# Optimization experiments

Hardware: AMD Instinct MI355X
Metric: run time of the kernel (lower is better)

The kernel has to match this reference:

```python
import jax, jax.numpy as jnp
import numpy as np

SIGMA = 5.67e-8  # Stefan-Boltzmann constant
NX = 13
N = NX * NX  # 169 nodes
B = 131072


def _build_matrices(L=0.1, thickness=0.001, board_k=15.0, emis=0.8):
    dx = L / (NX - 1)
    dy = L / (NX - 1)
    GLx = thickness * board_k * dy / dx
    GLy = thickness * board_k * dx / dy
    GR = 2.0 * dx * dy * emis
    iface = {0, NX - 1, NX * NX - 1, NX * NX - NX}
    K = np.zeros((N, N), dtype=np.float32)
    for j in range(NX):
        for i in range(NX):
            idn = i + NX * j
            if idn in iface:
                K[idn, idn] = 1.0
            else:
                gii = 0.0
                if i + 1 < NX:
                    K[idn, idn + 1] = -GLx  # east
                    gii += GLx
                if i - 1 >= 0:
                    K[idn, idn - 1] = -GLx  # west
                    gii += GLx
                if j + 1 < NX:
                    K[idn, idn + NX] = -GLx  # north (original code uses -GLx here too)
                    gii += GLy
                if j - 1 >= 0:
                    K[idn, idn - NX] = -GLx  # south (original code uses -GLx here too)
                    gii += GLy
                K[idn, idn] = gii
    e = np.full(N, GR, dtype=np.float32)
    for t in iface:
        e[t] = 0.0
    return jnp.asarray(K), jnp.asarray(e)


def setup_inputs() -> dict:
    key = jax.random.key(0)
    k1, k2, k3, k4 = jax.random.split(key, 4)
    # realistic temperatures (K) and heat loads (W)
    outputs = 270.0 + 60.0 * jax.random.uniform(k1, (B, NX, NX), dtype=jnp.float32)
    heaters = 0.5 * jax.random.uniform(k2, (B, NX, NX), dtype=jnp.float32)
    interfaces = 0.5 * jax.random.uniform(k3, (B, NX, NX), dtype=jnp.float32)
    Tenv = 270.0 + 30.0 * jax.random.uniform(k4, (B, 1), dtype=jnp.float32)
    K, e_diag = _build_matrices()
    return {"outputs": outputs, "heaters": heaters, "interfaces": interfaces,
            "Tenv": Tenv, "K": K, "e_diag": e_diag}


def reference(outputs, heaters, interfaces, Tenv, K, e_diag):
    b = outputs.shape[0]
    T = outputs.reshape(b, -1)                    # [B, 169]
    Q = heaters.reshape(b, -1) + interfaces.reshape(b, -1)  # [B, 169]
    # original computes K @ T_nodes_x_batch; batch-major equivalent is T @ K^T
    conduction = jnp.einsum('bn,mn->bm', T, K)    # [B, 169]
    radiation = SIGMA * e_diag[None, :] * (T ** 4 - Tenv ** 4)  # Tenv [B,1] broadcasts
    excess = conduction + radiation - Q
    return jnp.mean(jnp.abs(excess))
```

## Files before the change

kernel.cpp:

```cpp
#include <hip/hip_runtime.h>
#include <math.h>


#define SIGMA_F 5.67e-8f

constexpr int BLOCK = 256;

typedef float f4a __attribute__((ext_vector_type(4), aligned(4)));
typedef float f4b __attribute__((ext_vector_type(4), aligned(16)));

__global__ __launch_bounds__(256) void fused_residual_v4(
    const float* __restrict__ T,
    const float* __restrict__ H,
    const float* __restrict__ F,
    const float* __restrict__ Tenv,
    const float* __restrict__ K,
    const float* __restrict__ Ediag,
    float* __restrict__ partials,
    int total)
{
    __shared__ float sred[BLOCK / 64];

    const float GLx = -K[1 * 169 + 2];
    const float GRs = SIGMA_F * Ediag[1];

    const int lane = threadIdx.x & 63;
    float acc = 0.0f;

    const int gstride = gridDim.x * BLOCK;
    for (int g = blockIdx.x * BLOCK + threadIdx.x; g * 8 < total; g += gstride) {
        const int e0 = g * 8;
        const int waveBase = e0 - lane * 8;
        const bool fast = (waveBase >= 16) && (waveBase + 64 * 8 + 16 <= total);

        if (fast) {
            f4b t0 = *(const f4b*)(T + e0);
            f4b t1 = *(const f4b*)(T + e0 + 4);
            f4b h0 = __builtin_nontemporal_load((const f4b*)(H + e0));
            f4b h1 = __builtin_nontemporal_load((const f4b*)(H + e0 + 4));
            f4b f0 = __builtin_nontemporal_load((const f4b*)(F + e0));
            f4b f1 = __builtin_nontemporal_load((const f4b*)(F + e0 + 4));

            float sv[8];
            sv[0] = __shfl_up(t0.w, 2);
            sv[1] = __shfl_up(t1.x, 2);
            sv[2] = __shfl_up(t1.y, 2);
            sv[3] = __shfl_up(t1.z, 2);
            sv[4] = __shfl_up(t1.w, 2);
            sv[5] = __shfl_up(t0.x, 1);
            sv[6] = __shfl_up(t0.y, 1);
            sv[7] = __shfl_up(t0.z, 1);
            if (lane < 2) {
                f4a a = *(const f4a*)(T + e0 - 13);
                f4a b = *(const f4a*)(T + e0 - 9);
                sv[0] = a.x; sv[1] = a.y; sv[2] = a.z; sv[3] = a.w;
                sv[4] = b.x; sv[5] = b.y; sv[6] = b.z; sv[7] = b.w;
            }
            float nv[8];
            nv[0] = __shfl_down(t1.y, 1);
            nv[1] = __shfl_down(t1.z, 1);
            nv[2] = __shfl_down(t1.w, 1);
            nv[3] = __shfl_down(t0.x, 2);
            nv[4] = __shfl_down(t0.y, 2);
            nv[5] = __shfl_down(t0.z, 2);
            nv[6] = __shfl_down(t0.w, 2);
            nv[7] = __shfl_down(t1.x, 2);
            if (lane >= 62) {
                f4a a = *(const f4a*)(T + e0 + 13);
                f4a b = *(const f4a*)(T + e0 + 17);
                nv[0] = a.x; nv[1] = a.y; nv[2] = a.z; nv[3] = a.w;
                nv[4] = b.x; nv[5] = b.y; nv[6] = b.z; nv[7] = b.w;
            }
            float left = __shfl_up(t1.w, 1);
            if (lane == 0) left = T[e0 - 1];
            float right = __shfl_down(t0.x, 1);
            if (lane == 63) right = T[e0 + 8];

            unsigned ue = (unsigned)e0;
            unsigned b0 = ue / 169u;
            int m0 = (int)(ue - b0 * 169u);
            unsigned q13 = (unsigned)m0 / 13u;
            int i0 = m0 - (int)q13 * 13;

            float tvA = Tenv[b0];
            float tvB = tvA;
            if (m0 >= 162) tvB = Tenv[b0 + 1];
            float tv4A = (tvA * tvA) * (tvA * tvA);
            float tv4B = (tvB * tvB) * (tvB * tvB);

            const float tC[8] = {t0.x, t0.y, t0.z, t0.w, t1.x, t1.y, t1.z, t1.w};
            const float tW[8] = {left, t0.x, t0.y, t0.z, t0.w, t1.x, t1.y, t1.z};
            const float tE[8] = {t0.y, t0.z, t0.w, t1.x, t1.y, t1.z, t1.w, right};
            const float hq[8] = {h0.x + f0.x, h0.y + f0.y, h0.z + f0.z, h0.w + f0.w,
                                 h1.x + f1.x, h1.y + f1.y, h1.z + f1.z, h1.w + f1.w};

            int m = m0, ii = i0;
            bool wrapped = false;
            #pragma unroll
            for (int j = 0; j < 8; ++j) {
                float t = tC[j];
                bool cE = (ii < 12), cW = (ii > 0), cN = (m < 156), cS = (m >= 13);
                bool ifc = (m == 0) | (m == 12) | (m == 156) | (m == 168);
                float s  = (cE ? tE[j] : 0.0f) + (cW ? tW[j] : 0.0f)
                         + (cN ? nv[j] : 0.0f) + (cS ? sv[j] : 0.0f);
                float nn = (cE ? 1.0f : 0.0f) + (cW ? 1.0f : 0.0f)
                         + (cN ? 1.0f : 0.0f) + (cS ? 1.0f : 0.0f);
                float t2 = t * t, t4 = t2 * t2;
                float tv4 = wrapped ? tv4B : tv4A;
                float ex = ifc ? (t - hq[j])
                               : (GLx * (nn * t - s) + GRs * (t4 - tv4) - hq[j]);
                acc += fabsf(ex);
                ++m; ++ii;
                if (ii == 13) ii = 0;
                if (m == 169) { m = 0; ii = 0; wrapped = true; }
            }
        } else {
            #pragma unroll
            for (int j = 0; j < 8; ++j) {
                int e = e0 + j;
                if (e >= total) break;
                unsigned b = (unsigned)e / 169u;
                int m = e - (int)b * 169;
                unsigned q13 = (unsigned)m / 13u;
                int ii = m - (int)q13 * 13;
                bool cE = (ii < 12), cW = (ii > 0), cN = (m < 156), cS = (m >= 13);
                bool ifc = (m == 0) | (m == 12) | (m == 156) | (m == 168);
                float t  = T[e];
                float tEv = cE ? T[e + 1]  : 0.0f;
                float tWv = cW ? T[e - 1]  : 0.0f;
                float tNv = cN ? T[e + 13] : 0.0f;
                float tSv = cS ? T[e - 13] : 0.0f;
                float s  = tEv + tWv + tNv + tSv;
                float nn = (float)((int)cE + (int)cW + (int)cN + (int)cS);
                float tv = Tenv[b];
                float tv4 = (tv * tv) * (tv * tv);
                float t2 = t * t, t4 = t2 * t2;
                float q = H[e] + F[e];
                float ex = ifc ? (t - q)
                               : (GLx * (nn * t - s) + GRs * (t4 - tv4) - q);
                acc += fabsf(ex);
            }
        }
    }

    #pragma unroll
    for (int off = 32; off > 0; off >>= 1)
        acc += __shfl_down(acc, off, 64);
    int wid = threadIdx.x >> 6;
    if (lane == 0) sred[wid] = acc;
    __syncthreads();
    if (threadIdx.x == 0) {
        float s = 0.0f;
        #pragma unroll
        for (int w = 0; w < BLOCK / 64; ++w) s += sred[w];
        partials[blockIdx.x] = s;
    }
}

__global__ __launch_bounds__(256) void finalize_kernel(
    const float* __restrict__ partials, int n,
    float* __restrict__ out, float inv_total)
{
    __shared__ float sred[BLOCK / 64];
    float acc = 0.0f;
    for (int i = (int)threadIdx.x; i < n; i += BLOCK) acc += partials[i];
    #pragma unroll
    for (int off = 32; off > 0; off >>= 1)
        acc += __shfl_down(acc, off, 64);
    int lane = threadIdx.x & 63;
    int wid  = threadIdx.x >> 6;
    if (lane == 0) sred[wid] = acc;
    __syncthreads();
    if (threadIdx.x == 0) {
        float s = 0.0f;
        #pragma unroll
        for (int w = 0; w < BLOCK / 64; ++w) s += sred[w];
        out[0] = s * inv_total;
    }
}

extern "C" void kernel_launch(void* const* d_in, const int* in_sizes, int n_in,
                              void* d_out, int out_size, void* d_ws, size_t ws_size,
                              hipStream_t stream) {
    const float* T    = (const float*)d_in[0];
    const float* H    = (const float*)d_in[1];
    const float* F    = (const float*)d_in[2];
    const float* Tenv = (const float*)d_in[3];
    const float* K    = (const float*)d_in[4];
    const float* E    = (const float*)d_in[5];
    float* out      = (float*)d_out;
    float* partials = (float*)d_ws;

    const int total = in_sizes[0];

    int grid = (total / 8 + BLOCK - 1) / BLOCK;
    if ((size_t)grid * sizeof(float) > ws_size) grid = (int)(ws_size / sizeof(float));
    if (grid < 1) grid = 1;

    fused_residual_v4<<<grid, BLOCK, 0, stream>>>(T, H, F, Tenv, K, E, partials, total);

    const float inv_total = 1.0f / (float)total;
    finalize_kernel<<<1, BLOCK, 0, stream>>>(partials, grid, out, inv_total);
}
```

Baseline: 245.7 us.

## Assign one 13-element grid row per thread with direct neighbor-row loads

```diff
diff --git a/kernel.cpp b/kernel.cpp
--- a/kernel.cpp
+++ b/kernel.cpp
@@ -7,9 +7,8 @@
 constexpr int BLOCK = 256;
 
 typedef float f4a __attribute__((ext_vector_type(4), aligned(4)));
-typedef float f4b __attribute__((ext_vector_type(4), aligned(16)));
 
-__global__ __launch_bounds__(256) void fused_residual_v4(
+__global__ __launch_bounds__(256) void fused_residual_v5(
     const float* __restrict__ T,
     const float* __restrict__ H,
     const float* __restrict__ F,
@@ -17,136 +16,106 @@
     const float* __restrict__ K,
     const float* __restrict__ Ediag,
     float* __restrict__ partials,
-    int total)
+    int rows)
 {
     __shared__ float sred[BLOCK / 64];
 
     const float GLx = -K[1 * 169 + 2];
     const float GRs = SIGMA_F * Ediag[1];
 
-    const int lane = threadIdx.x & 63;
     float acc = 0.0f;
 
     const int gstride = gridDim.x * BLOCK;
-    for (int g = blockIdx.x * BLOCK + threadIdx.x; g * 8 < total; g += gstride) {
-        const int e0 = g * 8;
-        const int waveBase = e0 - lane * 8;
-        const bool fast = (waveBase >= 16) && (waveBase + 64 * 8 + 16 <= total);
+    for (int r = blockIdx.x * BLOCK + (int)threadIdx.x; r < rows; r += gstride) {
+        const unsigned ur = (unsigned)r;
+        const unsigned b  = ur / 13u;
+        const int j = (int)(ur - b * 13u);
+        const bool cS = (j > 0), cN = (j < 12);
+        const float fS = cS ? 1.0f : 0.0f;
+        const float fN = cN ? 1.0f : 0.0f;
 
-        if (fast) {
-            f4b t0 = *(const f4b*)(T + e0);
-            f4b t1 = *(const f4b*)(T + e0 + 4);
-            f4b h0 = __builtin_nontemporal_load((const f4b*)(H + e0));
-            f4b h1 = __builtin_nontemporal_load((const f4b*)(H + e0 + 4));
-            f4b f0 = __builtin_nontemporal_load((const f4b*)(F + e0));
-            f4b f1 = __builtin_nontemporal_load((const f4b*)(F + e0 + 4));
+        const int e0 = r * 13;
+        const float* Tp = T + e0;
+        const float* Sp = T + (cS ? e0 - 13 : e0);
+        const float* Np = T + (cN ? e0 + 13 : e0);
 
-            float sv[8];
-            sv[0] = __shfl_up(t0.w, 2);
-            sv[1] = __shfl_up(t1.x, 2);
-            sv[2] = __shfl_up(t1.y, 2);
-            sv[3] = __shfl_up(t1.z, 2);
-            sv[4] = __shfl_up(t1.w, 2);
-            sv[5] = __shfl_up(t0.x, 1);
-            sv[6] = __shfl_up(t0.y, 1);
-            sv[7] = __shfl_up(t0.z, 1);
-            if (lane < 2) {
-                f4a a = *(const f4a*)(T + e0 - 13);
-                f4a b = *(const f4a*)(T + e0 - 9);
-                sv[0] = a.x; sv[1] = a.y; sv[2] = a.z; sv[3] = a.w;
-                sv[4] = b.x; sv[5] = b.y; sv[6] = b.z; sv[7] = b.w;
-            }
-            float nv[8];
-            nv[0] = __shfl_down(t1.y, 1);
-            nv[1] = __shfl_down(t1.z, 1);
-            nv[2] = __shfl_down(t1.w, 1);
-            nv[3] = __shfl_down(t0.x, 2);
-            nv[4] = __shfl_down(t0.y, 2);
-            nv[5] = __shfl_down(t0.z, 2);
-            nv[6] = __shfl_down(t0.w, 2);
-            nv[7] = __shfl_down(t1.x, 2);
-            if (lane >= 62) {
-                f4a a = *(const f4a*)(T + e0 + 13);
-                f4a b = *(const f4a*)(T + e0 + 17);
-                nv[0] = a.x; nv[1] = a.y; nv[2] = a.z; nv[3] = a.w;
-                nv[4] = b.x; nv[5] = b.y; nv[6] = b.z; nv[7] = b.w;
-            }
-            float left = __shfl_up(t1.w, 1);
-            if (lane == 0) left = T[e0 - 1];
-            float right = __shfl_down(t0.x, 1);
-            if (lane == 63) right = T[e0 + 8];
+        f4a tA = *(const f4a*)(Tp);
+        f4a tB = *(const f4a*)(Tp + 4);
+        f4a tC = *(const f4a*)(Tp + 8);
+        float t12 = Tp[12];
+        f4a sA = *(const f4a*)(Sp);
+        f4a sB = *(const f4a*)(Sp + 4);
+        f4a sC = *(const f4a*)(Sp + 8);
+        float s12 = Sp[12];
+        f4a nA = *(const f4a*)(Np);
+        f4a nB = *(const f4a*)(Np + 4);
+        f4a nC = *(const f4a*)(Np + 8);
+        float n12 = Np[12];
+        f4a hA = __builtin_nontemporal_load((const f4a*)(H + e0));
+        f4a hB = __builtin_nontemporal_load((const f4a*)(H + e0 + 4));
+        f4a hC = __builtin_nontemporal_load((const f4a*)(H + e0 + 8));
+        float h12 = __builtin_nontemporal_load(H + e0 + 12);
+        f4a fA = __builtin_nontemporal_load((const f4a*)(F + e0));
+        f4a fB = __builtin_nontemporal_load((const f4a*)(F + e0 + 4));
+        f4a fC = __builtin_nontemporal_load((const f4a*)(F + e0 + 8));
+        float f12 = __builtin_nontemporal_load(F + e0 + 12);
 
-            unsigned ue = (unsigned)e0;
-            unsigned b0 = ue / 169u;
-            int m0 = (int)(ue - b0 * 169u);
-            unsigned q13 = (unsigned)m0 / 13u;
-            int i0 = m0 - (int)q13 * 13;
+        const float tv  = Tenv[b];
+        const float tv2 = tv * tv;
+        const float nGtv4 = -(GRs * (tv2 * tv2));
 
-            float tvA = Tenv[b0];
-            float tvB = tvA;
-            if (m0 >= 162) tvB = Tenv[b0 + 1];
-            float tv4A = (tvA * tvA) * (tvA * tvA);
-            float tv4B = (tvB * tvB) * (tvB * tvB);
+        const float tR[13] = {tA.x, tA.y, tA.z, tA.w, tB.x, tB.y, tB.z, tB.w,
+                              tC.x, tC.y, tC.z, tC.w, t12};
+        const float sR[13] = {sA.x, sA.y, sA.z, sA.w, sB.x, sB.y, sB.z, sB.w,
+                              sC.x, sC.y, sC.z, sC.w, s12};
+        const float nR[13] = {nA.x, nA.y, nA.z, nA.w, nB.x, nB.y, nB.z, nB.w,
+                              nC.x, nC.y, nC.z, nC.w, n12};
+        const float qR[13] = {hA.x + fA.x, hA.y + fA.y, hA.z + fA.z, hA.w + fA.w,
+                              hB.x + fB.x, hB.y + fB.y, hB.z + fB.z, hB.w + fB.w,
+                              hC.x + fC.x, hC.y + fC.y, hC.z + fC.z, hC.w + fC.w,
+                              h12 + f12};
 
-            const float tC[8] = {t0.x, t0.y, t0.z, t0.w, t1.x, t1.y, t1.z, t1.w};
-            const float tW[8] = {left, t0.x, t0.y, t0.z, t0.w, t1.x, t1.y, t1.z};
-            const float tE[8] = {t0.y, t0.z, t0.w, t1.x, t1.y, t1.z, t1.w, right};
-            const float hq[8] = {h0.x + f0.x, h0.y + f0.y, h0.z + f0.z, h0.w + f0.w,
-                                 h1.x + f1.x, h1.y + f1.y, h1.z + f1.z, h1.w + f1.w};
+        const float nnI = 2.0f + fN + fS;
+        const float nnE = 1.0f + fN + fS;
+        const bool ifc = (j == 0) | (j == 12);
 
-            int m = m0, ii = i0;
-            bool wrapped = false;
-            #pragma unroll
-            for (int j = 0; j < 8; ++j) {
-                float t = tC[j];
-                bool cE = (ii < 12), cW = (ii > 0), cN = (m < 156), cS = (m >= 13);
-                bool ifc = (m == 0) | (m == 12) | (m == 156) | (m == 168);
-                float s  = (cE ? tE[j] : 0.0f) + (cW ? tW[j] : 0.0f)
-                         + (cN ? nv[j] : 0.0f) + (cS ? sv[j] : 0.0f);
-                float nn = (cE ? 1.0f : 0.0f) + (cW ? 1.0f : 0.0f)
-                         + (cN ? 1.0f : 0.0f) + (cS ? 1.0f : 0.0f);
-                float t2 = t * t, t4 = t2 * t2;
-                float tv4 = wrapped ? tv4B : tv4A;
-                float ex = ifc ? (t - hq[j])
-                               : (GLx * (nn * t - s) + GRs * (t4 - tv4) - hq[j]);
-                acc += fabsf(ex);
-                ++m; ++ii;
-                if (ii == 13) ii = 0;
-                if (m == 169) { m = 0; ii = 0; wrapped = true; }
-            }
-        } else {
-            #pragma unroll
-            for (int j = 0; j < 8; ++j) {
-                int e = e0 + j;
-                if (e >= total) break;
-                unsigned b = (unsigned)e / 169u;
-                int m = e - (int)b * 169;
-                unsigned q13 = (unsigned)m / 13u;
-                int ii = m - (int)q13 * 13;
-                bool cE = (ii < 12), cW = (ii > 0), cN = (m < 156), cS = (m >= 13);
-                bool ifc = (m == 0) | (m == 12) | (m == 156) | (m == 168);
-                float t  = T[e];
-                float tEv = cE ? T[e + 1]  : 0.0f;
-                float tWv = cW ? T[e - 1]  : 0.0f;
-                float tNv = cN ? T[e + 13] : 0.0f;
-                float tSv = cS ? T[e - 13] : 0.0f;
-                float s  = tEv + tWv + tNv + tSv;
-                float nn = (float)((int)cE + (int)cW + (int)cN + (int)cS);
-                float tv = Tenv[b];
-                float tv4 = (tv * tv) * (tv * tv);
-                float t2 = t * t, t4 = t2 * t2;
-                float q = H[e] + F[e];
-                float ex = ifc ? (t - q)
-                               : (GLx * (nn * t - s) + GRs * (t4 - tv4) - q);
-                acc += fabsf(ex);
-            }
+        {
+            float t = tR[0];
+            float s = tR[1];
+            s = fmaf(fN, nR[0], s);
+            s = fmaf(fS, sR[0], s);
+            float t2 = t * t;
+            float ex = fmaf(GLx, fmaf(nnE, t, -s), fmaf(GRs, t2 * t2, nGtv4)) - qR[0];
+            float exI = t - qR[0];
+            acc += fabsf(ifc ? exI : ex);
+        }
+        #pragma unroll
+        for (int i = 1; i < 12; ++i) {
+            float t = tR[i];
+            float s = tR[i - 1] + tR[i + 1];
+            s = fmaf(fN, nR[i], s);
+            s = fmaf(fS, sR[i], s);
+            float t2 = t * t;
+            float ex = fmaf(GLx, fmaf(nnI, t, -s), fmaf(GRs, t2 * t2, nGtv4)) - qR[i];
+            acc += fabsf(ex);
+        }
+        {
+            float t = tR[12];
+            float s = tR[11];
+            s = fmaf(fN, nR[12], s);
+            s = fmaf(fS, sR[12], s);
+            float t2 = t * t;
+            float ex = fmaf(GLx, fmaf(nnE, t, -s), fmaf(GRs, t2 * t2, nGtv4)) - qR[12];
+            float exI = t - qR[12];
+            acc += fabsf(ifc ? exI : ex);
         }
     }
 
     #pragma unroll
     for (int off = 32; off > 0; off >>= 1)
         acc += __shfl_down(acc, off, 64);
-    int wid = threadIdx.x >> 6;
+    const int lane = threadIdx.x & 63;
+    const int wid  = threadIdx.x >> 6;
     if (lane == 0) sred[wid] = acc;
     __syncthreads();
     if (threadIdx.x == 0) {
@@ -192,12 +161,13 @@
     float* partials = (float*)d_ws;
 
     const int total = in_sizes[0];
+    const int rows  = total / 13;
 
-    int grid = (total / 8 + BLOCK - 1) / BLOCK;
+    int grid = (rows + BLOCK - 1) / BLOCK;
     if ((size_t)grid * sizeof(float) > ws_size) grid = (int)(ws_size / sizeof(float));
     if (grid < 1) grid = 1;
 
-    fused_residual_v4<<<grid, BLOCK, 0, stream>>>(T, H, F, Tenv, K, E, partials, total);
+    fused_residual_v5<<<grid, BLOCK, 0, stream>>>(T, H, F, Tenv, K, E, partials, rows);
 
     const float inv_total = 1.0f / (float)total;
     finalize_kernel<<<1, BLOCK, 0, stream>>>(partials, grid, out, inv_total);
```

Measured after the change: 275.0 us. 11.9% more time.
